# Kernel tuning notes

Measured on AMD Instinct MI355X. Metric: run time of the kernel, lower is better.

## Reference

```python
import jax, jax.numpy as jnp
import numpy as np

FUSION_RATIO = 0.1


def graph_conv(src, dst, x, W, b, n):
    # DGL GraphConv, norm='both': h = D_in^{-1/2} A D_out^{-1/2} (x W) + b
    ones = jnp.ones((src.shape[0],), x.dtype)
    deg_out = jnp.clip(jax.ops.segment_sum(ones, src, num_segments=n), 1.0)
    deg_in = jnp.clip(jax.ops.segment_sum(ones, dst, num_segments=n), 1.0)
    h = (x @ W) * (deg_out ** -0.5)[:, None]
    agg = jax.ops.segment_sum(h[src], dst, num_segments=n)  # [n, out]
    return agg * (deg_in ** -0.5)[:, None] + b


def norm_embed(e):
    # z-score (unbiased std, matching torch.std) then min-max
    e = (e - e.mean()) / jnp.std(e, ddof=1)
    return (e - e.min()) / (e.max() - e.min())


def setup_inputs() -> dict:
    key = jax.random.key(0)
    ks = jax.random.split(key, 24)
    n_apig, n_fcg = 50000, 100000
    e_apig, e_fcg = 800000, 1600000
    apig_dim, fcg_dim, hidden, united, ncls = 256, 128, 128, 64, 10
    s = 0.05
    inp = {
        'apig_feat': jax.random.normal(ks[0], (n_apig, apig_dim), jnp.float32),
        'fcg_feat': jax.random.normal(ks[1], (n_fcg, fcg_dim), jnp.float32),
        'W_a1': jax.random.normal(ks[2], (apig_dim, hidden), jnp.float32) * s,
        'b_a1': jnp.zeros((hidden,), jnp.float32),
        'W_a2': jax.random.normal(ks[3], (hidden, hidden), jnp.float32) * s,
        'b_a2': jnp.zeros((hidden,), jnp.float32),
        'W_f1': jax.random.normal(ks[4], (fcg_dim, hidden), jnp.float32) * s,
        'b_f1': jnp.zeros((hidden,), jnp.float32),
        'W_f2': jax.random.normal(ks[5], (hidden, hidden), jnp.float32) * s,
        'b_f2': jnp.zeros((hidden,), jnp.float32),
        'W1': jax.random.normal(ks[6], (hidden, united), jnp.float32) * s,
        'b1': jnp.zeros((united,), jnp.float32),
        'W2': jax.random.normal(ks[7], (united, hidden), jnp.float32) * s,
        'b2': jnp.zeros((hidden,), jnp.float32),
        'W_attn': jax.random.normal(ks[8], (hidden, 1), jnp.float32) * s,
        'b_attn': jnp.zeros((1,), jnp.float32),
        'W_cls': jax.random.normal(ks[9], (hidden, ncls), jnp.float32) * s,
        'b_cls': jnp.zeros((ncls,), jnp.float32),
        'apig_src': jax.random.randint(ks[10], (e_apig,), 0, n_apig, jnp.int32),
        'apig_dst': jax.random.randint(ks[11], (e_apig,), 0, n_apig, jnp.int32),
        'fcg_src': jax.random.randint(ks[12], (e_fcg,), 0, n_fcg, jnp.int32),
        'fcg_dst': jax.random.randint(ks[13], (e_fcg,), 0, n_fcg, jnp.int32),
        'n_apig': n_apig,
        'n_fcg': n_fcg,
    }
    return inp


def reference(apig_feat, fcg_feat, W_a1, b_a1, W_a2, b_a2, W_f1, b_f1, W_f2, b_f2,
              W1, b1, W2, b2, W_attn, b_attn, W_cls, b_cls,
              apig_src, apig_dst, fcg_src, fcg_dst, n_apig, n_fcg):
    h_a1 = jax.nn.relu(graph_conv(apig_src, apig_dst, apig_feat, W_a1, b_a1, n_apig))
    h_f1 = jax.nn.relu(graph_conv(fcg_src, fcg_dst, fcg_feat, W_f1, b_f1, n_fcg))
    a_enc = h_a1 @ W1 + b1
    f_enc = h_f1 @ W1 + b1
    a_sum = a_enc.sum(axis=0)
    f_sum = f_enc.sum(axis=0)
    a_enc = a_enc + FUSION_RATIO * f_sum
    f_enc = f_enc + FUSION_RATIO * a_sum
    a_dec = a_enc @ W2 + b2
    f_dec = f_enc @ W2 + b2
    h_a2 = jax.nn.relu(graph_conv(apig_src, apig_dst, a_dec, W_a2, b_a2, n_apig))
    h_f2 = jax.nn.relu(graph_conv(fcg_src, fcg_dst, f_dec, W_f2, b_f2, n_fcg))
    apig_emb = h_a2.mean(axis=0)  # dgl.mean_nodes, single graph -> [hidden]
    fcg_emb = h_f2.max(axis=0)    # dgl.max_nodes -> [hidden]
    a = norm_embed(apig_emb)
    f = norm_embed(fcg_emb)
    wa = jax.nn.softmax(a @ W_attn + b_attn, axis=0)  # [1] -> 1.0
    wf = jax.nn.softmax(f @ W_attn + b_attn, axis=0)
    emb = a * wa + f * wf
    # dropout is identity at inference
    return emb @ W_cls + b_cls
```

## Files before the change

kernel.cpp:

```cpp
#include <hip/hip_runtime.h>
#include <math.h>


typedef __attribute__((ext_vector_type(8))) short bf16x8;
typedef __attribute__((ext_vector_type(8))) unsigned short u16x8;
typedef __attribute__((ext_vector_type(4))) float f32x4;

#define SORT_T 4096

static __device__ inline unsigned short f2bf(float f) {
  unsigned u = __float_as_uint(f);
  unsigned r = (u + 0x7fff + ((u >> 16) & 1)) >> 16;
  return (unsigned short)r;
}
static __device__ inline float bf2f(unsigned short h) {
  return __uint_as_float(((unsigned)h) << 16);
}

__global__ void zero_small_kernel(float* __restrict__ s0, float* __restrict__ s1, int ns,
                                  float* __restrict__ ea, unsigned* __restrict__ ef, int ne,
                                  int* __restrict__ offs_a, int* __restrict__ offs_src_a,
                                  int n_a, int e_a,
                                  int* __restrict__ offs_f, int* __restrict__ offs_src_f,
                                  int n_f, int e_f) {
  int i = threadIdx.x;
  if (i < ns) { s0[i] = 0.f; s1[i] = 0.f; }
  if (i < ne) { ea[i] = 0.f; ef[i] = 0u; }
  if (i == 0) {
    offs_a[n_a] = e_a;
    offs_src_a[n_a] = e_a;
    offs_f[n_f] = e_f;
    offs_src_f[n_f] = e_f;
  }
}

static __device__ inline int edge_key(const int* __restrict__ a_key,
                                      const int* __restrict__ f_key, int e_a, int i) {
  return (i < e_a) ? a_key[i] : (f_key[i - e_a] + 65536);
}

__global__ __launch_bounds__(256) void radix_hist_kernel(
    const int* __restrict__ a_key, const int* __restrict__ f_key, int e_a, int E,
    int* __restrict__ blkhist, int B) {
  __shared__ int h[512];
  for (int i = threadIdx.x; i < 512; i += 256) h[i] = 0;
  __syncthreads();
  int base = blockIdx.x * SORT_T;
  int end = base + SORT_T;
  if (end > E) end = E;
  for (int i = base + threadIdx.x; i < end; i += 256)
    atomicAdd(&h[edge_key(a_key, f_key, e_a, i) >> 9], 1);
  __syncthreads();
  for (int i = threadIdx.x; i < 512; i += 256) blkhist[i * B + blockIdx.x] = h[i];
}

__global__ __launch_bounds__(256) void cursor_kernel(int* __restrict__ blkhist, int B,
                                                     int* __restrict__ bintotal) {
  __shared__ int part[256];
  int* row = blkhist + (size_t)blockIdx.x * B;
  int C = (B + 255) / 256;
  int start = threadIdx.x * C;
  int end = start + C;
  if (end > B) end = B;
  int v[8];
  int s = 0;
  for (int j = start; j < end; ++j) {
    v[j - start] = row[j];
    s += v[j - start];
  }
  part[threadIdx.x] = s;
  __syncthreads();
  for (int o = 1; o < 256; o <<= 1) {
    int u = (threadIdx.x >= o) ? part[threadIdx.x - o] : 0;
    __syncthreads();
    part[threadIdx.x] += u;
    __syncthreads();
  }
  int run = part[threadIdx.x] - s;
  for (int j = start; j < end; ++j) {
    row[j] = run;
    run += v[j - start];
  }
  if (threadIdx.x == 255) bintotal[blockIdx.x] = part[255];
}

__global__ __launch_bounds__(256) void binscan_kernel(const int* __restrict__ bintotal,
                                                      int* __restrict__ binstart) {
  __shared__ int x[512];
  x[threadIdx.x] = bintotal[threadIdx.x];
  x[threadIdx.x + 256] = bintotal[threadIdx.x + 256];
  __syncthreads();
  for (int o = 1; o < 512; o <<= 1) {
    int i0 = threadIdx.x, i1 = threadIdx.x + 256;
    int v0 = (i0 >= o) ? x[i0 - o] : 0;
    int v1 = (i1 >= o) ? x[i1 - o] : 0;
    __syncthreads();
    x[i0] += v0;
    x[i1] += v1;
    __syncthreads();
  }
  binstart[threadIdx.x] = x[threadIdx.x] - bintotal[threadIdx.x];
  binstart[threadIdx.x + 256] = x[threadIdx.x + 256] - bintotal[threadIdx.x + 256];
}

__global__ __launch_bounds__(256) void scatter_dst_kernel(
    const int* __restrict__ a_key, const int* __restrict__ f_key,
    const int* __restrict__ a_pay, const int* __restrict__ f_pay,
    int e_a, int E, const int* __restrict__ blkhist, int B,
    const int* __restrict__ binstart, int* __restrict__ opack) {
  __shared__ int cur[512];
  int b = blockIdx.x;
  for (int bin = threadIdx.x; bin < 512; bin += 256)
    cur[bin] = binstart[bin] + blkhist[bin * B + b];
  __syncthreads();
  int base = b * SORT_T;
  int end = base + SORT_T;
  if (end > E) end = E;
  for (int i = base + threadIdx.x; i < end; i += 256) {
    int k = edge_key(a_key, f_key, e_a, i);
    int pay = (i < e_a) ? a_pay[i] : f_pay[i - e_a];
    int pos = atomicAdd(&cur[k >> 9], 1);
    opack[pos] = ((k & 511) << 17) | pay;
  }
}

__global__ __launch_bounds__(256) void scatter_src_kernel(
    const int* __restrict__ a_key, const int* __restrict__ f_key,
    int e_a, int E, const int* __restrict__ blkhist, int B,
    const int* __restrict__ binstart, unsigned short* __restrict__ okey) {
  __shared__ int cur[512];
  int b = blockIdx.x;
  for (int bin = threadIdx.x; bin < 512; bin += 256)
    cur[bin] = binstart[bin] + blkhist[bin * B + b];
  __syncthreads();
  int base = b * SORT_T;
  int end = base + SORT_T;
  if (end > E) end = E;
  for (int i = base + threadIdx.x; i < end; i += 256) {
    int k = edge_key(a_key, f_key, e_a, i);
    int pos = atomicAdd(&cur[k >> 9], 1);
    okey[pos] = (unsigned short)(k & 511);
  }
}

__global__ __launch_bounds__(256) void bucket_dst_kernel(
    const int* __restrict__ kp, const int* __restrict__ binstart, int E, int e_a,
    int* __restrict__ csr, int* __restrict__ offs_a, int n_a,
    int* __restrict__ offs_f, int n_f) {
  __shared__ int h[512], x[512], cur[512];
  int b = blockIdx.x;
  int s = binstart[b];
  int e = (b == 511) ? E : binstart[b + 1];
  for (int i = threadIdx.x; i < 512; i += 256) h[i] = 0;
  __syncthreads();
  for (int i = s + threadIdx.x; i < e; i += 256) atomicAdd(&h[kp[i] >> 17], 1);
  __syncthreads();
  for (int i = threadIdx.x; i < 512; i += 256) x[i] = h[i];
  __syncthreads();
  for (int o = 1; o < 512; o <<= 1) {
    int i0 = threadIdx.x, i1 = threadIdx.x + 256;
    int v0 = (i0 >= o) ? x[i0 - o] : 0;
    int v1 = (i1 >= o) ? x[i1 - o] : 0;
    __syncthreads();
    x[i0] += v0;
    x[i1] += v1;
    __syncthreads();
  }
  for (int low = threadIdx.x; low < 512; low += 256) {
    int gpos = s + x[low] - h[low];
    cur[low] = gpos;
    int key = (b << 9) | low;
    if (key < 65536) {
      if (key < n_a) offs_a[key] = gpos;
    } else {
      int v = key - 65536;
      if (v < n_f) offs_f[v] = gpos - e_a;
    }
  }
  __syncthreads();
  for (int i = s + threadIdx.x; i < e; i += 256) {
    int pv = kp[i];
    int pos = atomicAdd(&cur[pv >> 17], 1);
    csr[pos] = pv & 0x1FFFF;
  }
}

__global__ __launch_bounds__(256) void bucket_src_kernel(
    const unsigned short* __restrict__ kl, const int* __restrict__ binstart, int E, int e_a,
    int* __restrict__ offs_src_a, int n_a, int* __restrict__ offs_src_f, int n_f) {
  __shared__ int h[512], x[512];
  int b = blockIdx.x;
  int s = binstart[b];
  int e = (b == 511) ? E : binstart[b + 1];
  for (int i = threadIdx.x; i < 512; i += 256) h[i] = 0;
  __syncthreads();
  for (int i = s + threadIdx.x; i < e; i += 256) atomicAdd(&h[kl[i]], 1);
  __syncthreads();
  for (int i = threadIdx.x; i < 512; i += 256) x[i] = h[i];
  __syncthreads();
  for (int o = 1; o < 512; o <<= 1) {
    int i0 = threadIdx.x, i1 = threadIdx.x + 256;
    int v0 = (i0 >= o) ? x[i0 - o] : 0;
    int v1 = (i1 >= o) ? x[i1 - o] : 0;
    __syncthreads();
    x[i0] += v0;
    x[i1] += v1;
    __syncthreads();
  }
  for (int low = threadIdx.x; low < 512; low += 256) {
    int gpos = s + x[low] - h[low];
    int key = (b << 9) | low;
    if (key < 65536) {
      if (key < n_a) offs_src_a[key] = gpos;
    } else {
      int v = key - 65536;
      if (v < n_f) offs_src_f[v] = gpos - e_a;
    }
  }
}

__global__ void isr_kernel(const int* __restrict__ offs_a, const int* __restrict__ offs_src_a,
                           float* __restrict__ io_a, float* __restrict__ ii_a, int n_a,
                           const int* __restrict__ offs_f, const int* __restrict__ offs_src_f,
                           float* __restrict__ io_f, float* __restrict__ ii_f, int n_f) {
  int i = blockIdx.x * blockDim.x + threadIdx.x;
  if (i < n_a) {
    int ci = offs_a[i + 1] - offs_a[i];
    int co = offs_src_a[i + 1] - offs_src_a[i];
    ii_a[i] = 1.0f / sqrtf((float)(ci < 1 ? 1 : ci));
    io_a[i] = 1.0f / sqrtf((float)(co < 1 ? 1 : co));
  }
  if (i < n_f) {
    int ci = offs_f[i + 1] - offs_f[i];
    int co = offs_src_f[i + 1] - offs_src_f[i];
    ii_f[i] = 1.0f / sqrtf((float)(ci < 1 ? 1 : ci));
    io_f[i] = 1.0f / sqrtf((float)(co < 1 ? 1 : co));
  }
}

#define LDT 72
__global__ __launch_bounds__(256) void gemm_mfma_kernel(
    const void* __restrict__ A, const float* __restrict__ B, void* __restrict__ C,
    int M, int N, int K,
    const float* __restrict__ add_vec, float add_scale,
    const float* __restrict__ rowscale, const float* __restrict__ bias,
    int in_bf16, int out_bf16) {
  __shared__ __align__(16) short As[64 * LDT];
  __shared__ __align__(16) short Bs[64 * LDT];
  const int m0 = blockIdx.x * 64, n0 = blockIdx.y * 64;
  const int tid = threadIdx.x;
  const int lane = tid & 63, w = tid >> 6;
  const int q = lane >> 4, l16 = lane & 15;
  const int srow = tid >> 2, schunk = (tid & 3) * 16;
  f32x4 acc[4] = {};
  for (int k0 = 0; k0 < K; k0 += 64) {
    {
      int m = m0 + srow;
      float tmp[16];
      if (m < M) {
        if (in_bf16) {
          const unsigned short* s = (const unsigned short*)A + (size_t)m * K + k0 + schunk;
          u16x8 v0 = *reinterpret_cast<const u16x8*>(s);
          u16x8 v1 = *reinterpret_cast<const u16x8*>(s + 8);
#pragma unroll
          for (int i = 0; i < 8; ++i) {
            tmp[i] = bf2f(v0[i]);
            tmp[8 + i] = bf2f(v1[i]);
          }
        } else {
          const float* s = (const float*)A + (size_t)m * K + k0 + schunk;
#pragma unroll
          for (int i = 0; i < 16; i += 4) {
            float4 v = *reinterpret_cast<const float4*>(s + i);
            tmp[i] = v.x; tmp[i + 1] = v.y; tmp[i + 2] = v.z; tmp[i + 3] = v.w;
          }
        }
        if (add_vec) {
#pragma unroll
          for (int i = 0; i < 16; ++i) tmp[i] += add_scale * add_vec[k0 + schunk + i];
        }
      } else {
#pragma unroll
        for (int i = 0; i < 16; ++i) tmp[i] = 0.f;
      }
#pragma unroll
      for (int i = 0; i < 16; ++i) As[srow * LDT + schunk + i] = (short)f2bf(tmp[i]);
    }
    {
      const float* s = B + (size_t)(k0 + srow) * N + n0 + schunk;
#pragma unroll
      for (int i = 0; i < 16; i += 4) {
        float4 v = *reinterpret_cast<const float4*>(s + i);
        Bs[(schunk + i + 0) * LDT + srow] = (short)f2bf(v.x);
        Bs[(schunk + i + 1) * LDT + srow] = (short)f2bf(v.y);
        Bs[(schunk + i + 2) * LDT + srow] = (short)f2bf(v.z);
        Bs[(schunk + i + 3) * LDT + srow] = (short)f2bf(v.w);
      }
    }
    __syncthreads();
#pragma unroll
    for (int kk = 0; kk < 2; ++kk) {
      bf16x8 af = *reinterpret_cast<const bf16x8*>(&As[(w * 16 + l16) * LDT + kk * 32 + q * 8]);
#pragma unroll
      for (int nt = 0; nt < 4; ++nt) {
        bf16x8 bf = *reinterpret_cast<const bf16x8*>(&Bs[(nt * 16 + l16) * LDT + kk * 32 + q * 8]);
        acc[nt] = __builtin_amdgcn_mfma_f32_16x16x32_bf16(af, bf, acc[nt], 0, 0, 0);
      }
    }
    __syncthreads();
  }
#pragma unroll
  for (int nt = 0; nt < 4; ++nt) {
    int gcol = n0 + nt * 16 + l16;
    float bv = bias ? bias[gcol] : 0.f;
#pragma unroll
    for (int r = 0; r < 4; ++r) {
      int grow = m0 + w * 16 + q * 4 + r;
      if (grow < M) {
        float v = acc[nt][r];
        if (rowscale) v *= rowscale[grow];
        v += bv;
        if (out_bf16)
          ((unsigned short*)C)[(size_t)grow * N + gcol] = f2bf(v);
        else
          ((float*)C)[(size_t)grow * N + gcol] = v;
      }
    }
  }
}

__global__ __launch_bounds__(256) void agg_kernel(
    const unsigned short* __restrict__ XW, const int* __restrict__ offs,
    const int* __restrict__ csr, const float* __restrict__ isr_in,
    const float* __restrict__ bias, void* __restrict__ out, int n, int mode) {
  __shared__ float red[8][128];
  int lane = threadIdx.x & 31;
  int g = threadIdx.x >> 5;
  int node = blockIdx.x * 8 + g;
  float4 o = make_float4(0.f, 0.f, 0.f, 0.f);
  if (node < n) {
    int e0 = offs[node], e1 = offs[node + 1];
    float4 a0 = make_float4(0.f, 0.f, 0.f, 0.f);
    float4 a1 = a0, a2 = a0, a3 = a0;
    int e = e0;
    for (; e + 4 <= e1; e += 4) {
      int s0 = csr[e], s1 = csr[e + 1], s2 = csr[e + 2], s3 = csr[e + 3];
      ushort4 v0 = *reinterpret_cast<const ushort4*>(&XW[(size_t)s0 * 128 + lane * 4]);
      ushort4 v1 = *reinterpret_cast<const ushort4*>(&XW[(size_t)s1 * 128 + lane * 4]);
      ushort4 v2 = *reinterpret_cast<const ushort4*>(&XW[(size_t)s2 * 128 + lane * 4]);
      ushort4 v3 = *reinterpret_cast<const ushort4*>(&XW[(size_t)s3 * 128 + lane * 4]);
      a0.x += bf2f(v0.x); a0.y += bf2f(v0.y); a0.z += bf2f(v0.z); a0.w += bf2f(v0.w);
      a1.x += bf2f(v1.x); a1.y += bf2f(v1.y); a1.z += bf2f(v1.z); a1.w += bf2f(v1.w);
      a2.x += bf2f(v2.x); a2.y += bf2f(v2.y); a2.z += bf2f(v2.z); a2.w += bf2f(v2.w);
      a3.x += bf2f(v3.x); a3.y += bf2f(v3.y); a3.z += bf2f(v3.z); a3.w += bf2f(v3.w);
    }
    for (; e < e1; ++e) {
      int s = csr[e];
      ushort4 v = *reinterpret_cast<const ushort4*>(&XW[(size_t)s * 128 + lane * 4]);
      a0.x += bf2f(v.x); a0.y += bf2f(v.y); a0.z += bf2f(v.z); a0.w += bf2f(v.w);
    }
    float4 acc;
    acc.x = (a0.x + a1.x) + (a2.x + a3.x);
    acc.y = (a0.y + a1.y) + (a2.y + a3.y);
    acc.z = (a0.z + a1.z) + (a2.z + a3.z);
    acc.w = (a0.w + a1.w) + (a2.w + a3.w);
    float sc = isr_in[node];
    float4 b = *reinterpret_cast<const float4*>(&bias[lane * 4]);
    o.x = fmaxf(fmaf(acc.x, sc, b.x), 0.f);
    o.y = fmaxf(fmaf(acc.y, sc, b.y), 0.f);
    o.z = fmaxf(fmaf(acc.z, sc, b.z), 0.f);
    o.w = fmaxf(fmaf(acc.w, sc, b.w), 0.f);
  }
  if (mode == 0) {
    if (node < n) {
      ushort4 st;
      st.x = f2bf(o.x); st.y = f2bf(o.y); st.z = f2bf(o.z); st.w = f2bf(o.w);
      *reinterpret_cast<ushort4*>(&((unsigned short*)out)[(size_t)node * 128 + lane * 4]) = st;
    }
    return;
  }
  red[g][lane * 4 + 0] = o.x;
  red[g][lane * 4 + 1] = o.y;
  red[g][lane * 4 + 2] = o.z;
  red[g][lane * 4 + 3] = o.w;
  __syncthreads();
  if (threadIdx.x < 128) {
    float v = red[0][threadIdx.x];
    if (mode == 1) {
#pragma unroll
      for (int j = 1; j < 8; ++j) v += red[j][threadIdx.x];
    } else {
#pragma unroll
      for (int j = 1; j < 8; ++j) v = fmaxf(v, red[j][threadIdx.x]);
    }
    ((float*)out)[(size_t)blockIdx.x * 128 + threadIdx.x] = v;
  }
}

__global__ __launch_bounds__(256) void colsum_kernel(const void* __restrict__ X,
                                                     float* __restrict__ out, int n, int ncol,
                                                     int xbf16) {
  __shared__ float s[256];
  int col = threadIdx.x % ncol;
  int rpb = 256 / ncol;
  int rb = threadIdx.x / ncol;
  float acc = 0.f;
  for (int r = blockIdx.x * rpb + rb; r < n; r += gridDim.x * rpb) {
    size_t idx = (size_t)r * ncol + col;
    acc += xbf16 ? bf2f(((const unsigned short*)X)[idx]) : ((const float*)X)[idx];
  }
  s[threadIdx.x] = acc;
  __syncthreads();
  if (threadIdx.x < ncol) {
    float v = 0.f;
    for (int i = 0; i < rpb; ++i) v += s[threadIdx.x + i * ncol];
    atomicAdd(&out[col], v);
  }
}

__global__ __launch_bounds__(256) void colmax_kernel(const float* __restrict__ X,
                                                     unsigned* __restrict__ out, int n, int ncol) {
  __shared__ float s[256];
  int col = threadIdx.x % ncol;
  int rpb = 256 / ncol;
  int rb = threadIdx.x / ncol;
  float acc = 0.f;
  for (int r = blockIdx.x * rpb + rb; r < n; r += gridDim.x * rpb)
    acc = fmaxf(acc, X[(size_t)r * ncol + col]);
  s[threadIdx.x] = acc;
  __syncthreads();
  if (threadIdx.x < ncol) {
    float v = s[threadIdx.x];
    for (int i = 1; i < rpb; ++i) v = fmaxf(v, s[threadIdx.x + i * ncol]);
    atomicMax(&out[col], __float_as_uint(v));
  }
}

__global__ __launch_bounds__(128) void final_kernel(
    const float* __restrict__ emb_a_sum, const unsigned* __restrict__ emb_f_bits,
    const float* __restrict__ W_cls, const float* __restrict__ b_cls,
    float* __restrict__ out, float inv_n_apig, int ncls) {
  __shared__ float red[128];
  __shared__ float emb[128];
  int t = threadIdx.x;
  float a = emb_a_sum[t] * inv_n_apig;
  float f = __uint_as_float(emb_f_bits[t]);

  float vals[2] = {a, f};
  float norms[2];
#pragma unroll
  for (int which = 0; which < 2; ++which) {
    float x = vals[which];
    red[t] = x;
    __syncthreads();
    for (int o = 64; o > 0; o >>= 1) {
      if (t < o) red[t] += red[t + o];
      __syncthreads();
    }
    float mean = red[0] / 128.f;
    __syncthreads();
    float d = x - mean;
    red[t] = d * d;
    __syncthreads();
    for (int o = 64; o > 0; o >>= 1) {
      if (t < o) red[t] += red[t + o];
      __syncthreads();
    }
    float stdv = sqrtf(red[0] / 127.f);
    __syncthreads();
    float z = d / stdv;
    red[t] = z;
    __syncthreads();
    for (int o = 64; o > 0; o >>= 1) {
      if (t < o) red[t] = fminf(red[t], red[t + o]);
      __syncthreads();
    }
    float zmin = red[0];
    __syncthreads();
    red[t] = z;
    __syncthreads();
    for (int o = 64; o > 0; o >>= 1) {
      if (t < o) red[t] = fmaxf(red[t], red[t + o]);
      __syncthreads();
    }
    float zmax = red[0];
    __syncthreads();
    norms[which] = (z - zmin) / (zmax - zmin);
  }

  emb[t] = norms[0] + norms[1];
  __syncthreads();
  if (t < ncls) {
    float acc = b_cls[t];
    for (int k = 0; k < 128; ++k) acc = fmaf(emb[k], W_cls[k * ncls + t], acc);
    out[t] = acc;
  }
}

extern "C" void kernel_launch(void* const* d_in, const int* in_sizes, int n_in,
                              void* d_out, int out_size, void* d_ws, size_t ws_size,
                              hipStream_t stream) {
  const float* apig_feat = (const float*)d_in[0];
  const float* fcg_feat = (const float*)d_in[1];
  const float* W_a1 = (const float*)d_in[2];
  const float* b_a1 = (const float*)d_in[3];
  const float* W_a2 = (const float*)d_in[4];
  const float* b_a2 = (const float*)d_in[5];
  const float* W_f1 = (const float*)d_in[6];
  const float* b_f1 = (const float*)d_in[7];
  const float* W_f2 = (const float*)d_in[8];
  const float* b_f2 = (const float*)d_in[9];
  const float* W1 = (const float*)d_in[10];
  const float* b1 = (const float*)d_in[11];
  const float* W2 = (const float*)d_in[12];
  const float* b2 = (const float*)d_in[13];
  const float* W_cls = (const float*)d_in[16];
  const float* b_cls = (const float*)d_in[17];
  const int* a_src = (const int*)d_in[18];
  const int* a_dst = (const int*)d_in[19];
  const int* f_src = (const int*)d_in[20];
  const int* f_dst = (const int*)d_in[21];

  const int hidden = in_sizes[3];
  const int united = in_sizes[11];
  const int ncls = in_sizes[17];
  const int apig_dim = in_sizes[2] / hidden;
  const int fcg_dim = in_sizes[6] / hidden;
  const int n_a = in_sizes[0] / apig_dim;
  const int n_f = in_sizes[1] / fcg_dim;
  const int e_a = in_sizes[18];
  const int e_f = in_sizes[20];

  char* w = (char*)d_ws;
  auto alloc = [&](size_t bytes) -> void* {
    void* p = (void*)w;
    w += (bytes + 255) & ~(size_t)255;
    return p;
  };
  const int E_tot = e_a + e_f;
  const int B = (E_tot + SORT_T - 1) / SORT_T;
  const int nblkA = (n_a + 7) / 8, nblkF = (n_f + 7) / 8;

  float* isr_out_a = (float*)alloc((size_t)n_a * 4);
  float* isr_in_a = (float*)alloc((size_t)n_a * 4);
  float* isr_out_f = (float*)alloc((size_t)n_f * 4);
  float* isr_in_f = (float*)alloc((size_t)n_f * 4);
  int* offs_a = (int*)alloc((size_t)(n_a + 1) * 4);
  int* offs_f = (int*)alloc((size_t)(n_f + 1) * 4);
  int* offs_src_a = (int*)alloc((size_t)(n_a + 1) * 4);
  int* offs_src_f = (int*)alloc((size_t)(n_f + 1) * 4);
  int* kp = (int*)alloc((size_t)E_tot * 4);
  int* csr = (int*)alloc((size_t)E_tot * 4);
  int* blkhist = (int*)alloc((size_t)512 * B * 4);
  int* bintotal = (int*)alloc((size_t)512 * 4);
  int* binstart = (int*)alloc((size_t)512 * 4);
  unsigned short* G_a = (unsigned short*)alloc((size_t)n_a * hidden * 2);
  unsigned short* H_a = (unsigned short*)alloc((size_t)n_a * hidden * 2);
  unsigned short* G_f = (unsigned short*)alloc((size_t)n_f * hidden * 2);
  unsigned short* H_f = (unsigned short*)alloc((size_t)n_f * hidden * 2);
  float* P = (float*)alloc((size_t)nblkF * hidden * 4);
  unsigned short* E_a = G_a;
  unsigned short* E_f = G_f;
  float* a_sum = (float*)alloc((size_t)united * 4);
  float* f_sum = (float*)alloc((size_t)united * 4);
  float* emb_a = (float*)alloc((size_t)hidden * 4);
  unsigned* emb_f = (unsigned*)alloc((size_t)hidden * 4);
  int* csr_a = csr;
  int* csr_f = csr + e_a;
  unsigned short* ks = (unsigned short*)kp;
  (void)ws_size;
  (void)n_in;
  (void)out_size;

  dim3 blk(256);

  zero_small_kernel<<<1, 128, 0, stream>>>(a_sum, f_sum, united, emb_a, emb_f, hidden,
                                           offs_a, offs_src_a, n_a, e_a,
                                           offs_f, offs_src_f, n_f, e_f);

  radix_hist_kernel<<<B, blk, 0, stream>>>(a_dst, f_dst, e_a, E_tot, blkhist, B);
  cursor_kernel<<<512, blk, 0, stream>>>(blkhist, B, bintotal);
  binscan_kernel<<<1, blk, 0, stream>>>(bintotal, binstart);
  scatter_dst_kernel<<<B, blk, 0, stream>>>(a_dst, f_dst, a_src, f_src, e_a, E_tot,
                                            blkhist, B, binstart, kp);
  bucket_dst_kernel<<<512, blk, 0, stream>>>(kp, binstart, E_tot, e_a,
                                             csr, offs_a, n_a, offs_f, n_f);
  radix_hist_kernel<<<B, blk, 0, stream>>>(a_src, f_src, e_a, E_tot, blkhist, B);
  cursor_kernel<<<512, blk, 0, stream>>>(blkhist, B, bintotal);
  binscan_kernel<<<1, blk, 0, stream>>>(bintotal, binstart);
  scatter_src_kernel<<<B, blk, 0, stream>>>(a_src, f_src, e_a, E_tot, blkhist, B,
                                            binstart, ks);
  bucket_src_kernel<<<512, blk, 0, stream>>>(ks, binstart, E_tot, e_a,
                                             offs_src_a, n_a, offs_src_f, n_f);
  isr_kernel<<<(n_f + 255) / 256, blk, 0, stream>>>(offs_a, offs_src_a, isr_out_a, isr_in_a,
                                                    n_a, offs_f, offs_src_f, isr_out_f,
                                                    isr_in_f, n_f);

  const int ga = (n_a + 63) / 64, gf = (n_f + 63) / 64;

  gemm_mfma_kernel<<<dim3(ga, hidden / 64), blk, 0, stream>>>(
      apig_feat, W_a1, G_a, n_a, hidden, apig_dim, nullptr, 0.f, isr_out_a, nullptr, 0, 1);
  agg_kernel<<<nblkA, blk, 0, stream>>>(G_a, offs_a, csr_a, isr_in_a, b_a1, H_a, n_a, 0);
  gemm_mfma_kernel<<<dim3(ga, united / 64), blk, 0, stream>>>(
      H_a, W1, E_a, n_a, united, hidden, nullptr, 0.f, nullptr, b1, 1, 1);
  colsum_kernel<<<256, blk, 0, stream>>>(E_a, a_sum, n_a, united, 1);

  gemm_mfma_kernel<<<dim3(gf, hidden / 64), blk, 0, stream>>>(
      fcg_feat, W_f1, G_f, n_f, hidden, fcg_dim, nullptr, 0.f, isr_out_f, nullptr, 0, 1);
  agg_kernel<<<nblkF, blk, 0, stream>>>(G_f, offs_f, csr_f, isr_in_f, b_f1, H_f, n_f, 0);
  gemm_mfma_kernel<<<dim3(gf, united / 64), blk, 0, stream>>>(
      H_f, W1, E_f, n_f, united, hidden, nullptr, 0.f, nullptr, b1, 1, 1);
  colsum_kernel<<<256, blk, 0, stream>>>(E_f, f_sum, n_f, united, 1);

  gemm_mfma_kernel<<<dim3(ga, hidden / 64), blk, 0, stream>>>(
      E_a, W2, H_a, n_a, hidden, united, f_sum, 0.1f, nullptr, b2, 1, 1);
  gemm_mfma_kernel<<<dim3(ga, hidden / 64), blk, 0, stream>>>(
      H_a, W_a2, G_a, n_a, hidden, hidden, nullptr, 0.f, isr_out_a, nullptr, 1, 1);
  agg_kernel<<<nblkA, blk, 0, stream>>>(G_a, offs_a, csr_a, isr_in_a, b_a2, P, n_a, 1);
  colsum_kernel<<<256, blk, 0, stream>>>(P, emb_a, nblkA, hidden, 0);

  gemm_mfma_kernel<<<dim3(gf, hidden / 64), blk, 0, stream>>>(
      E_f, W2, H_f, n_f, hidden, united, a_sum, 0.1f, nullptr, b2, 1, 1);
  gemm_mfma_kernel<<<dim3(gf, hidden / 64), blk, 0, stream>>>(
      H_f, W_f2, G_f, n_f, hidden, hidden, nullptr, 0.f, isr_out_f, nullptr, 1, 1);
  agg_kernel<<<nblkF, blk, 0, stream>>>(G_f, offs_f, csr_f, isr_in_f, b_f2, P, n_f, 2);
  colmax_kernel<<<256, blk, 0, stream>>>(P, emb_f, nblkF, hidden);

  final_kernel<<<1, 128, 0, stream>>>(emb_a, emb_f, W_cls, b_cls, (float*)d_out,
                                      1.0f / (float)n_a, ncls);
}
```

Measured before the change: 710.5 us.

## Pre-transpose weights to bf16 and use LDS-free direct-load MFMA GEMM

Adds a prep kernel that converts each weight matrix once per call to a transposed bf16 layout. The LDS-staged tiled GEMM is replaced by a templated kernel where each wave loads A fragments directly from global memory and B fragments from the small transposed weights. Each block now covers the full output width, so A is read once instead of once per 64-column tile, and LDS barriers and per-tile fp32-to-bf16 weight conversion go away. The risk is that B fragments now come from global/L2 rather than LDS, and there is one extra launch.

```diff
diff --git a/kernel.cpp b/kernel.cpp
--- a/kernel.cpp
+++ b/kernel.cpp
@@ -34,6 +34,31 @@
   }
 }
 
+__global__ __launch_bounds__(256) void prep_bt_kernel(
+    const float* __restrict__ W_a1, const float* __restrict__ W_f1,
+    const float* __restrict__ W_a2, const float* __restrict__ W_f2,
+    const float* __restrict__ W1, const float* __restrict__ W2,
+    unsigned short* __restrict__ T_a1, unsigned short* __restrict__ T_f1,
+    unsigned short* __restrict__ T_a2, unsigned short* __restrict__ T_f2,
+    unsigned short* __restrict__ T1, unsigned short* __restrict__ T2) {
+  const float* src;
+  unsigned short* dst;
+  int K, N;
+  switch (blockIdx.y) {
+    case 0: src = W_a1; dst = T_a1; K = 256; N = 128; break;
+    case 1: src = W_f1; dst = T_f1; K = 128; N = 128; break;
+    case 2: src = W_a2; dst = T_a2; K = 128; N = 128; break;
+    case 3: src = W_f2; dst = T_f2; K = 128; N = 128; break;
+    case 4: src = W1;   dst = T1;   K = 128; N = 64;  break;
+    default: src = W2;  dst = T2;   K = 64;  N = 128; break;
+  }
+  int total = K * N;
+  for (int idx = blockIdx.x * 256 + threadIdx.x; idx < total; idx += gridDim.x * 256) {
+    int n = idx / K, k = idx - n * K;
+    dst[idx] = f2bf(src[(size_t)k * N + n]);
+  }
+}
+
 static __device__ inline int edge_key(const int* __restrict__ a_key,
                                       const int* __restrict__ f_key, int e_a, int i) {
   return (i < e_a) ? a_key[i] : (f_key[i - e_a] + 65536);
@@ -238,80 +263,63 @@
   }
 }
 
-#define LDT 72
-__global__ __launch_bounds__(256) void gemm_mfma_kernel(
-    const void* __restrict__ A, const float* __restrict__ B, void* __restrict__ C,
-    int M, int N, int K,
+template <int K, int N>
+__global__ __launch_bounds__(256) void gemm_direct_kernel(
+    const void* __restrict__ A, const unsigned short* __restrict__ Bt,
+    void* __restrict__ C, int M,
     const float* __restrict__ add_vec, float add_scale,
     const float* __restrict__ rowscale, const float* __restrict__ bias,
     int in_bf16, int out_bf16) {
-  __shared__ __align__(16) short As[64 * LDT];
-  __shared__ __align__(16) short Bs[64 * LDT];
-  const int m0 = blockIdx.x * 64, n0 = blockIdx.y * 64;
   const int tid = threadIdx.x;
   const int lane = tid & 63, w = tid >> 6;
   const int q = lane >> 4, l16 = lane & 15;
-  const int srow = tid >> 2, schunk = (tid & 3) * 16;
-  f32x4 acc[4] = {};
-  for (int k0 = 0; k0 < K; k0 += 64) {
-    {
-      int m = m0 + srow;
-      float tmp[16];
-      if (m < M) {
-        if (in_bf16) {
-          const unsigned short* s = (const unsigned short*)A + (size_t)m * K + k0 + schunk;
-          u16x8 v0 = *reinterpret_cast<const u16x8*>(s);
-          u16x8 v1 = *reinterpret_cast<const u16x8*>(s + 8);
+  const int m0 = blockIdx.x * 64;
+  const int m = m0 + w * 16 + l16;
+  const int mload = (m < M) ? m : (M - 1);
+  constexpr int NT = N / 16;
+  f32x4 acc[NT] = {};
 #pragma unroll
-          for (int i = 0; i < 8; ++i) {
-            tmp[i] = bf2f(v0[i]);
-            tmp[8 + i] = bf2f(v1[i]);
-          }
-        } else {
-          const float* s = (const float*)A + (size_t)m * K + k0 + schunk;
+  for (int kk = 0; kk < K / 32; ++kk) {
+    const int kb = kk * 32 + q * 8;
+    bf16x8 af;
+    if (in_bf16) {
+      af = *reinterpret_cast<const bf16x8*>((const unsigned short*)A + (size_t)mload * K + kb);
+      if (add_vec) {
+        float4 av0 = *reinterpret_cast<const float4*>(add_vec + kb);
+        float4 av1 = *reinterpret_cast<const float4*>(add_vec + kb + 4);
+        u16x8 u = (u16x8)af;
+        bf16x8 t;
+        t[0] = (short)f2bf(bf2f(u[0]) + add_scale * av0.x);
+        t[1] = (short)f2bf(bf2f(u[1]) + add_scale * av0.y);
+        t[2] = (short)f2bf(bf2f(u[2]) + add_scale * av0.z);
+        t[3] = (short)f2bf(bf2f(u[3]) + add_scale * av0.w);
+        t[4] = (short)f2bf(bf2f(u[4]) + add_scale * av1.x);
+        t[5] = (short)f2bf(bf2f(u[5]) + add_scale * av1.y);
+        t[6] = (short)f2bf(bf2f(u[6]) + add_scale * av1.z);
+        t[7] = (short)f2bf(bf2f(u[7]) + add_scale * av1.w);
+        af = t;
+      }
+    } else {
+      const float* s = (const float*)A + (size_t)mload * K + kb;
+      float4 v0 = *reinterpret_cast<const float4*>(s);
+      float4 v1 = *reinterpret_cast<const float4*>(s + 4);
+      bf16x8 t;
+      t[0] = (short)f2bf(v0.x); t[1] = (short)f2bf(v0.y);
+      t[2] = (short)f2bf(v0.z); t[3] = (short)f2bf(v0.w);
+      t[4] = (short)f2bf(v1.x); t[5] = (short)f2bf(v1.y);
+      t[6] = (short)f2bf(v1.z); t[7] = (short)f2bf(v1.w);
+      af = t;
+    }
 #pragma unroll
-          for (int i = 0; i < 16; i += 4) {
-            float4 v = *reinterpret_cast<const float4*>(s + i);
-            tmp[i] = v.x; tmp[i + 1] = v.y; tmp[i + 2] = v.z; tmp[i + 3] = v.w;
-          }
-        }
-        if (add_vec) {
+    for (int nt = 0; nt < NT; ++nt) {
+      bf16x8 bf =
+          *reinterpret_cast<const bf16x8*>(Bt + (size_t)(nt * 16 + l16) * K + kb);
+      acc[nt] = __builtin_amdgcn_mfma_f32_16x16x32_bf16(af, bf, acc[nt], 0, 0, 0);
+    }
+  }
 #pragma unroll
-          for (int i = 0; i < 16; ++i) tmp[i] += add_scale * add_vec[k0 + schunk + i];
-        }
-      } else {
-#pragma unroll
-        for (int i = 0; i < 16; ++i) tmp[i] = 0.f;
-      }
-#pragma unroll
-      for (int i = 0; i < 16; ++i) As[srow * LDT + schunk + i] = (short)f2bf(tmp[i]);
-    }
-    {
-      const float* s = B + (size_t)(k0 + srow) * N + n0 + schunk;
-#pragma unroll
-      for (int i = 0; i < 16; i += 4) {
-        float4 v = *reinterpret_cast<const float4*>(s + i);
-        Bs[(schunk + i + 0) * LDT + srow] = (short)f2bf(v.x);
-        Bs[(schunk + i + 1) * LDT + srow] = (short)f2bf(v.y);
-        Bs[(schunk + i + 2) * LDT + srow] = (short)f2bf(v.z);
-        Bs[(schunk + i + 3) * LDT + srow] = (short)f2bf(v.w);
-      }
-    }
-    __syncthreads();
-#pragma unroll
-    for (int kk = 0; kk < 2; ++kk) {
-      bf16x8 af = *reinterpret_cast<const bf16x8*>(&As[(w * 16 + l16) * LDT + kk * 32 + q * 8]);
-#pragma unroll
-      for (int nt = 0; nt < 4; ++nt) {
-        bf16x8 bf = *reinterpret_cast<const bf16x8*>(&Bs[(nt * 16 + l16) * LDT + kk * 32 + q * 8]);
-        acc[nt] = __builtin_amdgcn_mfma_f32_16x16x32_bf16(af, bf, acc[nt], 0, 0, 0);
-      }
-    }
-    __syncthreads();
-  }
-#pragma unroll
-  for (int nt = 0; nt < 4; ++nt) {
-    int gcol = n0 + nt * 16 + l16;
+  for (int nt = 0; nt < NT; ++nt) {
+    int gcol = nt * 16 + l16;
     float bv = bias ? bias[gcol] : 0.f;
 #pragma unroll
     for (int r = 0; r < 4; ++r) {
@@ -565,6 +573,12 @@
   float* f_sum = (float*)alloc((size_t)united * 4);
   float* emb_a = (float*)alloc((size_t)hidden * 4);
   unsigned* emb_f = (unsigned*)alloc((size_t)hidden * 4);
+  unsigned short* T_a1 = (unsigned short*)alloc((size_t)apig_dim * hidden * 2);
+  unsigned short* T_f1 = (unsigned short*)alloc((size_t)fcg_dim * hidden * 2);
+  unsigned short* T_a2 = (unsigned short*)alloc((size_t)hidden * hidden * 2);
+  unsigned short* T_f2 = (unsigned short*)alloc((size_t)hidden * hidden * 2);
+  unsigned short* T1 = (unsigned short*)alloc((size_t)hidden * united * 2);
+  unsigned short* T2 = (unsigned short*)alloc((size_t)united * hidden * 2);
   int* csr_a = csr;
   int* csr_f = csr + e_a;
   unsigned short* ks = (unsigned short*)kp;
@@ -577,6 +591,8 @@
   zero_small_kernel<<<1, 128, 0, stream>>>(a_sum, f_sum, united, emb_a, emb_f, hidden,
                                            offs_a, offs_src_a, n_a, e_a,
                                            offs_f, offs_src_f, n_f, e_f);
+  prep_bt_kernel<<<dim3(32, 6), blk, 0, stream>>>(W_a1, W_f1, W_a2, W_f2, W1, W2,
+                                                  T_a1, T_f1, T_a2, T_f2, T1, T2);
 
   radix_hist_kernel<<<B, blk, 0, stream>>>(a_dst, f_dst, e_a, E_tot, blkhist, B);
   cursor_kernel<<<512, blk, 0, stream>>>(blkhist, B, bintotal);
@@ -598,31 +614,31 @@
 
   const int ga = (n_a + 63) / 64, gf = (n_f + 63) / 64;
 
-  gemm_mfma_kernel<<<dim3(ga, hidden / 64), blk, 0, stream>>>(
-      apig_feat, W_a1, G_a, n_a, hidden, apig_dim, nullptr, 0.f, isr_out_a, nullptr, 0, 1);
+  gemm_direct_kernel<256, 128><<<ga, blk, 0, stream>>>(
+      apig_feat, T_a1, G_a, n_a, nullptr, 0.f, isr_out_a, nullptr, 0, 1);
   agg_kernel<<<nblkA, blk, 0, stream>>>(G_a, offs_a, csr_a, isr_in_a, b_a1, H_a, n_a, 0);
-  gemm_mfma_kernel<<<dim3(ga, united / 64), blk, 0, stream>>>(
-      H_a, W1, E_a, n_a, united, hidden, nullptr, 0.f, nullptr, b1, 1, 1);
+  gemm_direct_kernel<128, 64><<<ga, blk, 0, stream>>>(
+      H_a, T1, E_a, n_a, nullptr, 0.f, nullptr, b1, 1, 1);
   colsum_kernel<<<256, blk, 0, stream>>>(E_a, a_sum, n_a, united, 1);
 
-  gemm_mfma_kernel<<<dim3(gf, hidden / 64), blk, 0, stream>>>(
-      fcg_feat, W_f1, G_f, n_f, hidden, fcg_dim, nullptr, 0.f, isr_out_f, nullptr, 0, 1);
+  gemm_direct_kernel<128, 128><<<gf, blk, 0, stream>>>(
+      fcg_feat, T_f1, G_f, n_f, nullptr, 0.f, isr_out_f, nullptr, 0, 1);
   agg_kernel<<<nblkF, blk, 0, stream>>>(G_f, offs_f, csr_f, isr_in_f, b_f1, H_f, n_f, 0);
-  gemm_mfma_kernel<<<dim3(gf, united / 64), blk, 0, stream>>>(
-      H_f, W1, E_f, n_f, united, hidden, nullptr, 0.f, nullptr, b1, 1, 1);
+  gemm_direct_kernel<128, 64><<<gf, blk, 0, stream>>>(
+      H_f, T1, E_f, n_f, nullptr, 0.f, nullptr, b1, 1, 1);
   colsum_kernel<<<256, blk, 0, stream>>>(E_f, f_sum, n_f, united, 1);
 
-  gemm_mfma_kernel<<<dim3(ga, hidden / 64), blk, 0, stream>>>(
-      E_a, W2, H_a, n_a, hidden, united, f_sum, 0.1f, nullptr, b2, 1, 1);
-  gemm_mfma_kernel<<<dim3(ga, hidden / 64), blk, 0, stream>>>(
-      H_a, W_a2, G_a, n_a, hidden, hidden, nullptr, 0.f, isr_out_a, nullptr, 1, 1);
+  gemm_direct_kernel<64, 128><<<ga, blk, 0, stream>>>(
+      E_a, T2, H_a, n_a, f_sum, 0.1f, nullptr, b2, 1, 1);
+  gemm_direct_kernel<128, 128><<<ga, blk, 0, stream>>>(
+      H_a, T_a2, G_a, n_a, nullptr, 0.f, isr_out_a, nullptr, 1, 1);
   agg_kernel<<<nblkA, blk, 0, stream>>>(G_a, offs_a, csr_a, isr_in_a, b_a2, P, n_a, 1);
   colsum_kernel<<<256, blk, 0, stream>>>(P, emb_a, nblkA, hidden, 0);
 
-  gemm_mfma_kernel<<<dim3(gf, hidden / 64), blk, 0, stream>>>(
-      E_f, W2, H_f, n_f, hidden, united, a_sum, 0.1f, nullptr, b2, 1, 1);
-  gemm_mfma_kernel<<<dim3(gf, hidden / 64), blk, 0, stream>>>(
-      H_f, W_f2, G_f, n_f, hidden, hidden, nullptr, 0.f, isr_out_f, nullptr, 1, 1);
+  gemm_direct_kernel<64, 128><<<gf, blk, 0, stream>>>(
+      E_f, T2, H_f, n_f, a_sum, 0.1f, nullptr, b2, 1, 1);
+  gemm_direct_kernel<128, 128><<<gf, blk, 0, stream>>>(
+      H_f, T_f2, G_f, n_f, nullptr, 0.f, isr_out_f, nullptr, 1, 1);
   agg_kernel<<<nblkF, blk, 0, stream>>>(G_f, offs_f, csr_f, isr_in_f, b_f2, P, n_f, 2);
   colmax_kernel<<<256, blk, 0, stream>>>(P, emb_f, nblkF, hidden);
 
```

New measurement: 806.1 us. +13.5%, slower.
